# Kernel optimization log

Hardware: AMD Instinct MI355X
Metric: run time of the kernel (lower is better)

## Reference

```python
import jax, jax.numpy as jnp
import numpy as np

B, D, H = 16, 512, 8
MA, MR = 2048, 256  # padded max atoms / residues per graph
EPS = 1e-5


def _counts():
    ca = 1024 + (np.arange(B) * 97) % 1024   # atoms per graph
    cr = 128 + (np.arange(B) * 37) % 128     # residues per graph
    return ca, cr


def to_dense(x, batch, M):
    """PyG to_dense_batch: flat [N, D] + sorted batch ids -> [B, M, D] padded + mask."""
    N = x.shape[0]
    counts = jax.ops.segment_sum(jnp.ones(N, jnp.int32), batch, num_segments=B)
    starts = jnp.concatenate([jnp.zeros(1, counts.dtype), jnp.cumsum(counts)[:-1]])
    pos = jnp.arange(N, dtype=jnp.int32) - starts[batch]
    dense = jnp.zeros((B, M, x.shape[1]), x.dtype).at[batch, pos].set(x)
    mask = jnp.zeros((B, M), bool).at[batch, pos].set(True)
    return dense, mask, batch, pos


def mha(q, k, v, in_w, in_b, out_w, out_b, key_valid):
    """torch nn.MultiheadAttention (batch_first, eval) with key_padding_mask = ~key_valid."""
    Lq, Lk = q.shape[1], k.shape[1]
    dh = D // H
    wq, wk, wv = in_w[:D], in_w[D:2 * D], in_w[2 * D:]
    bq, bk, bv = in_b[:D], in_b[D:2 * D], in_b[2 * D:]
    qh = (q @ wq.T + bq).reshape(B, Lq, H, dh)
    kh = (k @ wk.T + bk).reshape(B, Lk, H, dh)
    vh = (v @ wv.T + bv).reshape(B, Lk, H, dh)
    scores = jnp.einsum('bqhd,bkhd->bhqk', qh, kh) / jnp.sqrt(jnp.asarray(dh, q.dtype))
    scores = jnp.where(key_valid[:, None, None, :], scores, jnp.asarray(-1e9, scores.dtype))
    attn = jax.nn.softmax(scores, axis=-1)
    out = jnp.einsum('bhqk,bkhd->bqhd', attn, vh).reshape(B, Lq, D)
    return out @ out_w.T + out_b


def layernorm(x, g, b):
    m = x.mean(-1, keepdims=True)
    v = ((x - m) ** 2).mean(-1, keepdims=True)
    return (x - m) * jax.lax.rsqrt(v + EPS) * g + b


def setup_inputs() -> dict:
    key = jax.random.key(0)
    ks = jax.random.split(key, 8)
    ca, cr = _counts()
    Na, Nr = int(ca.sum()), int(cr.sum())
    s = 0.02
    return {
        'atom_node': jax.random.normal(ks[0], (Na, D), jnp.float32),
        'res_node': jax.random.normal(ks[1], (Nr, D), jnp.float32),
        'r2a_in_w': jax.random.normal(ks[2], (3 * D, D), jnp.float32) * s,
        'r2a_in_b': jnp.zeros((3 * D,), jnp.float32),
        'r2a_out_w': jax.random.normal(ks[3], (D, D), jnp.float32) * s,
        'r2a_out_b': jnp.zeros((D,), jnp.float32),
        'a2r_in_w': jax.random.normal(ks[4], (3 * D, D), jnp.float32) * s,
        'a2r_in_b': jnp.zeros((3 * D,), jnp.float32),
        'a2r_out_w': jax.random.normal(ks[5], (D, D), jnp.float32) * s,
        'a2r_out_b': jnp.zeros((D,), jnp.float32),
        'atom_ln_g': jnp.ones((D,), jnp.float32),
        'atom_ln_b': jnp.zeros((D,), jnp.float32),
        'res_ln_g': jnp.ones((D,), jnp.float32),
        'res_ln_b': jnp.zeros((D,), jnp.float32),
        'atom_batch': jnp.asarray(np.repeat(np.arange(B), ca), jnp.int32),
        'res_batch': jnp.asarray(np.repeat(np.arange(B), cr), jnp.int32),
    }


def reference(atom_node, res_node, r2a_in_w, r2a_in_b, r2a_out_w, r2a_out_b,
              a2r_in_w, a2r_in_b, a2r_out_w, a2r_out_b,
              atom_ln_g, atom_ln_b, res_ln_g, res_ln_b,
              atom_batch, res_batch):
    atom_d, atom_mask, ab, ap = to_dense(atom_node, atom_batch, MA)
    res_d, res_mask, rb, rp = to_dense(res_node, res_batch, MR)
    # res2atom: atoms attend over residues; atom2res: residues attend over (updated) atoms
    atom_upd = mha(atom_d, res_d, res_d, r2a_in_w, r2a_in_b, r2a_out_w, r2a_out_b, res_mask)
    res_upd = mha(res_d, atom_upd, atom_upd, a2r_in_w, a2r_in_b, a2r_out_w, a2r_out_b, atom_mask)
    atom_out = layernorm(atom_upd, atom_ln_g, atom_ln_b)[ab, ap] + atom_node
    res_out = layernorm(res_upd, res_ln_g, res_ln_b)[rb, rp] + res_node
    return atom_out, res_out
```

## Files before the change

kernel.cpp:

```cpp
#include <hip/hip_runtime.h>
#include <hip/hip_bf16.h>
#include <math.h>

#define DD 512
#define NA_TOT 22904
#define NR_TOT 2904
#define MPAD_A 22960
#define MPAD_R 2960

__constant__ int c_aoff[17] = {0,1024,2145,3363,4678,6090,7599,9205,10908,12708,
                               14605,16599,17666,18830,20091,21449,22904};
__constant__ int c_roff[17] = {0,128,293,495,734,882,1067,1289,1420,1588,
                               1793,2035,2186,2374,2599,2733,2904};
__constant__ int c_apad[17] = {0,1024,2152,3376,4696,6112,7624,9232,10936,12736,
                               14640,16640,17712,18880,20144,21504,22960};
__constant__ int c_rpad[17] = {0,128,296,504,744,896,1088,1312,1448,1616,
                               1824,2072,2224,2416,2648,2784,2960};

typedef __attribute__((ext_vector_type(8))) short short8;
typedef __attribute__((ext_vector_type(4))) float f32x4;
typedef __attribute__((ext_vector_type(4))) unsigned short ushort4v;

__device__ __forceinline__ unsigned short f2bf(float f) {
  __hip_bfloat16 h = __float2bfloat16(f);
  return *reinterpret_cast<unsigned short*>(&h);
}
__device__ __forceinline__ float bf2f(unsigned short u) {
  union { unsigned int i; float f; } c; c.i = ((unsigned int)u) << 16; return c.f;
}
__device__ __forceinline__ float wred_sum(float x){
#pragma unroll
  for (int o = 32; o > 0; o >>= 1) x += __shfl_xor(x, o, 64);
  return x;
}

__device__ __forceinline__ void gl_lds16(const unsigned short* g, unsigned short* l) {
  __builtin_amdgcn_global_load_lds(
      (const __attribute__((address_space(1))) unsigned int*)g,
      (__attribute__((address_space(3))) unsigned int*)l, 16, 0, 0);
}

__global__ __launch_bounds__(256) void cvt5(
    const float* __restrict__ s0, const float* __restrict__ s1,
    const float* __restrict__ s2, const float* __restrict__ s3,
    const float* __restrict__ s4,
    unsigned short* __restrict__ d0, unsigned short* __restrict__ d1,
    unsigned short* __restrict__ d2, unsigned short* __restrict__ d3,
    unsigned short* __restrict__ d4,
    int n0, int n1, int n2, int n3, int n4)
{
  const float* s; unsigned short* d; int n;
  switch (blockIdx.y) {
    case 0: s = s0; d = d0; n = n0; break;
    case 1: s = s1; d = d1; n = n1; break;
    case 2: s = s2; d = d2; n = n2; break;
    case 3: s = s3; d = d3; n = n3; break;
    default: s = s4; d = d4; n = n4; break;
  }
  const int i = (blockIdx.x * 256 + threadIdx.x) * 4;
  if (i < n) {
    const float4 v = *reinterpret_cast<const float4*>(s + i);
    ushort4v o = { f2bf(v.x), f2bf(v.y), f2bf(v.z), f2bf(v.w) };
    *reinterpret_cast<ushort4v*>(d + i) = o;
  }
}

__global__ __launch_bounds__(256) void cvt_atom(const float* __restrict__ s,
                                                unsigned short* __restrict__ d, int n)
{
  const int i = (blockIdx.x * 256 + threadIdx.x) * 8;
  if (i < n) {
    const float4 v0 = *reinterpret_cast<const float4*>(s + i);
    const float4 v1 = *reinterpret_cast<const float4*>(s + i + 4);
    short8 pk;
    pk[0] = (short)f2bf(v0.x); pk[1] = (short)f2bf(v0.y);
    pk[2] = (short)f2bf(v0.z); pk[3] = (short)f2bf(v0.w);
    pk[4] = (short)f2bf(v1.x); pk[5] = (short)f2bf(v1.y);
    pk[6] = (short)f2bf(v1.z); pk[7] = (short)f2bf(v1.w);
    *reinterpret_cast<short8*>(d + i) = pk;
  }
}

__global__ __launch_bounds__(256) void mkmap(int* __restrict__ mapA,
                                             int* __restrict__ mapR)
{
  const int pm = blockIdx.x * 256 + threadIdx.x;
  if (pm < MPAD_A) {
    int b = 0;
#pragma unroll
    for (int i = 1; i < 16; ++i) if (pm >= c_apad[i]) b = i;
    const int rel = pm - c_apad[b];
    const int L = c_aoff[b+1] - c_aoff[b];
    mapA[pm] = c_aoff[b] + min(rel, L - 1);
  }
  if (pm < MPAD_R) {
    int b = 0;
#pragma unroll
    for (int i = 1; i < 16; ++i) if (pm >= c_rpad[i]) b = i;
    const int rel = pm - c_rpad[b];
    const int L = c_roff[b+1] - c_roff[b];
    mapR[pm] = c_roff[b] + min(rel, L - 1);
  }
}

struct GSeg {
  const void* X; const unsigned short* W; const float* bias;
  unsigned short* Y; const int* map;
  int M; int ldY; int mtiles; int flags;
};
struct GSeg4 { GSeg s[4]; };

__global__ __launch_bounds__(256) void gemm_multi(GSeg4 P, int mtpx)
{
  __shared__ unsigned short SMEM[40960];
  unsigned short* const Xb0 = SMEM;
  unsigned short* const Xb1 = SMEM + 8192;
  unsigned short* const Xb2 = SMEM + 16384;
  unsigned short* const Wb0 = SMEM + 24576;
  unsigned short* const Wb1 = SMEM + 32768;
  const GSeg sg = P.s[blockIdx.y];
  const int xcd = blockIdx.x & 7, g = blockIdx.x >> 3;
  const int mt = xcd + 8 * (g % mtpx);
  const int nt = g / mtpx;
  if (mt >= sg.mtiles) return;
  const int m0 = mt * 128, n0 = nt * 128;
  const int OUTT = sg.flags & 2, REMAP = sg.flags & 4;
  const int tid = threadIdx.x, lane = tid & 63, w = tid >> 6;
  const int la = lane & 15, lg = lane >> 4;
  const int wm = (w & 1) * 64, wn = (w >> 1) * 64;
  const int w64 = w * 64;
  const unsigned short* Xg = (const unsigned short*)sg.X;

  f32x4 acc[4][4];
#pragma unroll
  for (int i = 0; i < 4; ++i)
#pragma unroll
    for (int j = 0; j < 4; ++j) acc[i][j] = (f32x4){0.f,0.f,0.f,0.f};

  int elA[4][2], elB[4][2];
#pragma unroll
  for (int i = 0; i < 4; ++i)
#pragma unroll
    for (int kc = 0; kc < 2; ++kc) {
      { const int r = wm + i*16 + la;
        elA[i][kc] = r*64 + ((kc*32 + lg*8) ^ ((r & 7) << 3)); }
      { const int r = wn + i*16 + la;
        elB[i][kc] = r*64 + ((kc*32 + lg*8) ^ ((r & 7) << 3)); }
    }

  int srow[4];
#pragma unroll
  for (int p = 0; p < 4; ++p) {
    const int slot = p*256 + tid;
    const int rg = min(m0 + (slot >> 3), sg.M - 1);
    srow[p] = REMAP ? sg.map[rg] : rg;
  }
  int scg[4], srw[4];
#pragma unroll
  for (int p = 0; p < 4; ++p) {
    const int slot = p*256 + tid;
    srw[p] = slot >> 3;
    scg[p] = ((slot & 7) ^ (srw[p] & 7)) << 3;
  }

#define STAGE_W(DST, kb_)                                                       \
  _Pragma("unroll")                                                             \
  for (int p = 0; p < 4; ++p)                                                   \
    gl_lds16(sg.W + (size_t)(n0 + srw[p]) * DD + (kb_) + scg[p],                \
             &(DST)[(p*256 + w64) * 8]);

#define STAGE_X(DST, kb_)                                                       \
  _Pragma("unroll")                                                             \
  for (int p = 0; p < 4; ++p)                                                   \
    gl_lds16(Xg + (size_t)srow[p] * DD + (kb_) + scg[p],                        \
             &(DST)[(p*256 + w64) * 8]);

#define COMPUTE(XB, WB)                                                         \
  {                                                                             \
    short8 af[4][2], bfm[4][2];                                                 \
    _Pragma("unroll")                                                           \
    for (int i = 0; i < 4; ++i)                                                 \
      _Pragma("unroll")                                                         \
      for (int kc = 0; kc < 2; ++kc) {                                          \
        af[i][kc]  = *reinterpret_cast<const short8*>(&(XB)[elA[i][kc]]);       \
        bfm[i][kc] = *reinterpret_cast<const short8*>(&(WB)[elB[i][kc]]);       \
      }                                                                         \
    _Pragma("unroll")                                                           \
    for (int kc = 0; kc < 2; ++kc)                                              \
      _Pragma("unroll")                                                         \
      for (int i = 0; i < 4; ++i)                                               \
        _Pragma("unroll")                                                       \
        for (int j = 0; j < 4; ++j)                                             \
          acc[i][j] = __builtin_amdgcn_mfma_f32_16x16x32_bf16(af[i][kc], bfm[j][kc], acc[i][j], 0, 0, 0); \
  }

  STAGE_W(Wb0, 0);
  STAGE_X(Xb0, 0);
  STAGE_X(Xb1, 64);

#pragma unroll
  for (int k = 0; k < 8; ++k) {
    __builtin_amdgcn_s_barrier();
    asm volatile("" ::: "memory");
    if (k + 1 < 8) {
      if (((k+1) & 1) == 0) { STAGE_W(Wb0, (k+1)*64); } else { STAGE_W(Wb1, (k+1)*64); }
    }
    if (k + 2 < 8) {
      if (((k+2) % 3) == 0) { STAGE_X(Xb0, (k+2)*64); }
      else if (((k+2) % 3) == 1) { STAGE_X(Xb1, (k+2)*64); }
      else { STAGE_X(Xb2, (k+2)*64); }
    }
    if (k < 6)       { asm volatile("s_waitcnt vmcnt(12)" ::: "memory"); }
    else if (k == 6) { asm volatile("s_waitcnt vmcnt(8)" ::: "memory"); }
    else             { asm volatile("s_waitcnt vmcnt(0)" ::: "memory"); }
    __builtin_amdgcn_s_barrier();
    asm volatile("" ::: "memory");
    __builtin_amdgcn_sched_barrier(0);
    if ((k % 3) == 0)      { if ((k & 1) == 0) COMPUTE(Xb0, Wb0) else COMPUTE(Xb0, Wb1) }
    else if ((k % 3) == 1) { if ((k & 1) == 0) COMPUTE(Xb1, Wb0) else COMPUTE(Xb1, Wb1) }
    else                   { if ((k & 1) == 0) COMPUTE(Xb2, Wb0) else COMPUTE(Xb2, Wb1) }
  }

#undef STAGE_W
#undef STAGE_X
#undef COMPUTE

  __syncthreads();
  unsigned short* Cs = SMEM;
  if (!OUTT) {
#pragma unroll
    for (int j = 0; j < 4; ++j) {
      const int n = wn + j*16 + la;
      const float bj = sg.bias[n0 + n];
#pragma unroll
      for (int i = 0; i < 4; ++i) {
        const int mb = wm + i*16 + lg*4;
#pragma unroll
        for (int r = 0; r < 4; ++r) {
          const int m = mb + r;
          Cs[m*128 + (((n >> 3) ^ (m & 7)) << 3) + (n & 7)] = f2bf(acc[i][j][r] + bj);
        }
      }
    }
    __syncthreads();
#pragma unroll
    for (int p = 0; p < 8; ++p) {
      const int sid = p*256 + tid;
      const int row = sid >> 4, s = sid & 15;
      if (m0 + row < sg.M) {
        const short8 v = *reinterpret_cast<const short8*>(&Cs[row*128 + ((s ^ (row & 7)) << 3)]);
        *reinterpret_cast<short8*>(sg.Y + (size_t)(m0 + row)*sg.ldY + n0 + s*8) = v;
      }
    }
  } else {
#pragma unroll
    for (int j = 0; j < 4; ++j) {
      const int n = wn + j*16 + la;
      const float bj = sg.bias[n0 + n];
#pragma unroll
      for (int i = 0; i < 4; ++i) {
        const int mb = wm + i*16 + lg*4;
#pragma unroll
        for (int r = 0; r < 4; ++r) {
          const int m = mb + r;
          Cs[n*128 + (((m >> 3) ^ (n & 7)) << 3) + (m & 7)] = f2bf(acc[i][j][r] + bj);
        }
      }
    }
    __syncthreads();
#pragma unroll
    for (int p = 0; p < 8; ++p) {
      const int sid = p*256 + tid;
      const int row = sid >> 4, s = sid & 15;
      if (m0 + s*8 < sg.M) {
        const short8 v = *reinterpret_cast<const short8*>(&Cs[row*128 + ((s ^ (row & 7)) << 3)]);
        *reinterpret_cast<short8*>(sg.Y + (size_t)(n0 + row)*sg.ldY + m0 + s*8) = v;
      }
    }
  }
}

#define ATT_STAGE(bi, kc_)                                                      \
  {                                                                             \
    const int kbase_ = (kc_) * 64;                                              \
    _Pragma("unroll")                                                           \
    for (int p = 0; p < 2; ++p) {                                               \
      const int slot = p*256 + tid;                                             \
      const int row = slot >> 3, cg = slot & 7;                                 \
      const int srow = min(kbase_ + row, padL - 1);                             \
      gl_lds16(Kb + (size_t)srow * DD + ((cg ^ (row & 7)) << 3),                \
               &Ks[bi][(p*256 + w*64) * 8]);                                    \
    }                                                                           \
    _Pragma("unroll")                                                           \
    for (int p = 0; p < 2; ++p) {                                               \
      const int slot = p*256 + tid;                                             \
      const int row = slot >> 3, cg = slot & 7;                                 \
      const int col = min(kbase_ + ((cg ^ (row & 7)) << 3), padL - 8);          \
      gl_lds16(VTb + (size_t)row * ldvt + col, &Vs[bi][(p*256 + w*64) * 8]);    \
    }                                                                           \
  }

#define ATT_COMPUTE(bi, kbase)                                                  \
  {                                                                             \
    f32x4 S[4];                                                                 \
    _Pragma("unroll")                                                           \
    for (int j = 0; j < 4; ++j) {                                               \
      const int row = j*16 + la;                                                \
      const short8 kf0 = *reinterpret_cast<const short8*>(                      \
          &Ks[bi][row*64 + ((lg*8) ^ ((row & 7) << 3))]);                       \
      const short8 kf1 = *reinterpret_cast<const short8*>(                      \
          &Ks[bi][row*64 + ((32 + lg*8) ^ ((row & 7) << 3))]);                  \
      f32x4 s = (f32x4){0.f,0.f,0.f,0.f};                                       \
      s = __builtin_amdgcn_mfma_f32_16x16x32_bf16(qf[0], kf0, s, 0, 0, 0);      \
      s = __builtin_amdgcn_mfma_f32_16x16x32_bf16(qf[1], kf1, s, 0, 0, 0);      \
      S[j] = s;                                                                 \
    }                                                                           \
    _Pragma("unroll")                                                           \
    for (int j = 0; j < 4; ++j) {                                               \
      const bool ok = (kbase + j*16 + la) < Lk;                                 \
      _Pragma("unroll")                                                         \
      for (int r = 0; r < 4; ++r) {                                             \
        const float p = ok ? __expf(S[j][r] * 0.125f) : 0.f;                    \
        S[j][r] = p;                                                            \
        lsum[r] += p;                                                           \
      }                                                                         \
    }                                                                           \
    _Pragma("unroll")                                                           \
    for (int r = 0; r < 4; ++r) {                                               \
      const int prow = lg*4 + r;                                                \
      _Pragma("unroll")                                                         \
      for (int j = 0; j < 4; ++j)                                               \
        Pl[w][prow*64 + ((j*16 + la) ^ ((prow & 7) << 3))] = f2bf(S[j][r]);     \
    }                                                                           \
    __builtin_amdgcn_wave_barrier();                                            \
    const short8 pf0 = *reinterpret_cast<const short8*>(                        \
        &Pl[w][la*64 + ((lg*8) ^ ((la & 7) << 3))]);                            \
    const short8 pf1 = *reinterpret_cast<const short8*>(                        \
        &Pl[w][la*64 + ((32 + lg*8) ^ ((la & 7) << 3))]);                       \
    _Pragma("unroll")                                                           \
    for (int j = 0; j < 4; ++j) {                                               \
      const int d = j*16 + la;                                                  \
      const short8 vf0 = *reinterpret_cast<const short8*>(                      \
          &Vs[bi][d*64 + ((lg*8) ^ ((d & 7) << 3))]);                           \
      const short8 vf1 = *reinterpret_cast<const short8*>(                      \
          &Vs[bi][d*64 + ((32 + lg*8) ^ ((d & 7) << 3))]);                      \
      acc[j] = __builtin_amdgcn_mfma_f32_16x16x32_bf16(pf0, vf0, acc[j], 0, 0, 0); \
      acc[j] = __builtin_amdgcn_mfma_f32_16x16x32_bf16(pf1, vf1, acc[j], 0, 0, 0); \
    }                                                                           \
  }

__global__ __launch_bounds__(256, 4) void attn_v7(const unsigned short* __restrict__ Q,
                                                  const unsigned short* __restrict__ K,
                                                  const unsigned short* __restrict__ VT,
                                                  unsigned short* __restrict__ O, int ldvt)
{
  __shared__ unsigned short Ks[2][64*64];
  __shared__ unsigned short Vs[2][64*64];
  __shared__ unsigned short Pl[4][16*64];
  const int b = blockIdx.x >> 3, h = blockIdx.x & 7;
  const int Lq = c_aoff[b+1]-c_aoff[b], Lk = c_roff[b+1]-c_roff[b];
  const int padL = c_rpad[b+1]-c_rpad[b];
  const int q0b = blockIdx.y * 64;
  if (q0b >= Lq) return;
  const int tid = threadIdx.x, w = tid >> 6, lane = tid & 63;
  const int la = lane & 15, lg = lane >> 4;
  const int q0 = q0b + w*16;
  const unsigned short* Qb  = Q  + (size_t)c_aoff[b]*DD + h*64;
  const unsigned short* Kb  = K  + (size_t)c_rpad[b]*DD + h*64;
  const unsigned short* VTb = VT + (size_t)(h*64)*ldvt + c_rpad[b];

  short8 qf[2];
  {
    const int qrow = min(q0 + la, Lq - 1);
    qf[0] = *reinterpret_cast<const short8*>(Qb + (size_t)qrow*DD + lg*8);
    qf[1] = *reinterpret_cast<const short8*>(Qb + (size_t)qrow*DD + 32 + lg*8);
  }

  f32x4 acc[4];
#pragma unroll
  for (int j = 0; j < 4; ++j) acc[j] = (f32x4){0.f,0.f,0.f,0.f};
  float lsum[4] = {0.f,0.f,0.f,0.f};

  const int nkc = (Lk + 63) >> 6;
  ATT_STAGE(0, 0);
  for (int kc = 0; kc < nkc; ++kc) {
    const int bi = kc & 1;
    __builtin_amdgcn_s_barrier();
    asm volatile("" ::: "memory");
    if (kc + 1 < nkc) {
      ATT_STAGE(bi ^ 1, kc + 1);
      asm volatile("s_waitcnt vmcnt(4)" ::: "memory");
    } else {
      asm volatile("s_waitcnt vmcnt(0)" ::: "memory");
    }
    __builtin_amdgcn_s_barrier();
    asm volatile("" ::: "memory");
    __builtin_amdgcn_sched_barrier(0);
    const int kbase = kc * 64;
    ATT_COMPUTE(bi, kbase);
  }

#pragma unroll
  for (int msk = 1; msk <= 8; msk <<= 1)
#pragma unroll
    for (int r = 0; r < 4; ++r) lsum[r] += __shfl_xor(lsum[r], msk, 64);

#pragma unroll
  for (int r = 0; r < 4; ++r) {
    const float inv = 1.f / lsum[r];
    const int prow = lg*4 + r;
#pragma unroll
    for (int j = 0; j < 4; ++j)
      Pl[w][prow*64 + ((j*16 + la) ^ ((prow & 7) << 3))] = f2bf(acc[j][r] * inv);
  }
  __builtin_amdgcn_wave_barrier();
#pragma unroll
  for (int p = 0; p < 2; ++p) {
    const int sid = p*64 + lane;
    const int row = sid >> 3, s = sid & 7;
    const int qrow = q0 + row;
    if (qrow < Lq) {
      const short8 v = *reinterpret_cast<const short8*>(
          &Pl[w][row*64 + ((s ^ (row & 7)) << 3)]);
      *reinterpret_cast<short8*>(O + (size_t)(c_aoff[b] + qrow)*DD + h*64 + s*8) = v;
    }
  }
}

__global__ __launch_bounds__(256, 4) void attn_sk(const unsigned short* __restrict__ Q,
                                                  const unsigned short* __restrict__ K,
                                                  const unsigned short* __restrict__ VT,
                                                  float* __restrict__ Pout)
{
  __shared__ unsigned short Ks[2][64*64];
  __shared__ unsigned short Vs[2][64*64];
  __shared__ unsigned short Pl[4][16*64];
  const int b = blockIdx.x >> 3, h = blockIdx.x & 7;
  const int qt = blockIdx.y, z = blockIdx.z;
  const int Lq = c_roff[b+1]-c_roff[b], Lk = c_aoff[b+1]-c_aoff[b];
  const int padL = c_apad[b+1]-c_apad[b];
  const int ldvt = MPAD_A;
  const int q0b = qt * 64;
  if (q0b >= Lq) return;
  const int tid = threadIdx.x, w = tid >> 6, lane = tid & 63;
  const int la = lane & 15, lg = lane >> 4;
  const int q0 = q0b + w*16;
  float* pp = Pout + ((size_t)(blockIdx.x*4 + qt)*4 + z) * 4160;

  const int nkc = (Lk + 63) >> 6;
  const int cps = (nkc + 3) >> 2;
  const int k0 = z * cps, k1 = min(k0 + cps, nkc);
  if (k0 >= k1) {
    for (int i = tid; i < 4160; i += 256) pp[i] = 0.f;
    return;
  }

  const unsigned short* Qb  = Q  + (size_t)c_roff[b]*DD + h*64;
  const unsigned short* Kb  = K  + (size_t)c_apad[b]*DD + h*64;
  const unsigned short* VTb = VT + (size_t)(h*64)*ldvt + c_apad[b];

  short8 qf[2];
  {
    const int qrow = min(q0 + la, Lq - 1);
    qf[0] = *reinterpret_cast<const short8*>(Qb + (size_t)qrow*DD + lg*8);
    qf[1] = *reinterpret_cast<const short8*>(Qb + (size_t)qrow*DD + 32 + lg*8);
  }

  f32x4 acc[4];
#pragma unroll
  for (int j = 0; j < 4; ++j) acc[j] = (f32x4){0.f,0.f,0.f,0.f};
  float lsum[4] = {0.f,0.f,0.f,0.f};

  ATT_STAGE(0, k0);
  for (int kc = k0; kc < k1; ++kc) {
    const int bi = (kc - k0) & 1;
    __builtin_amdgcn_s_barrier();
    asm volatile("" ::: "memory");
    if (kc + 1 < k1) {
      ATT_STAGE(bi ^ 1, kc + 1);
      asm volatile("s_waitcnt vmcnt(4)" ::: "memory");
    } else {
      asm volatile("s_waitcnt vmcnt(0)" ::: "memory");
    }
    __builtin_amdgcn_s_barrier();
    asm volatile("" ::: "memory");
    __builtin_amdgcn_sched_barrier(0);
    const int kbase = kc * 64;
    ATT_COMPUTE(bi, kbase);
  }

#pragma unroll
  for (int msk = 1; msk <= 8; msk <<= 1)
#pragma unroll
    for (int r = 0; r < 4; ++r) lsum[r] += __shfl_xor(lsum[r], msk, 64);

#pragma unroll
  for (int j = 0; j < 4; ++j)
#pragma unroll
    for (int r = 0; r < 4; ++r)
      pp[(size_t)(w*16 + lg*4 + r)*64 + j*16 + la] = acc[j][r];
  if (la == 0) {
#pragma unroll
    for (int r = 0; r < 4; ++r) pp[4096 + w*16 + lg*4 + r] = lsum[r];
  }
}

__global__ __launch_bounds__(256) void attn_red(const float* __restrict__ Pin,
                                                unsigned short* __restrict__ O)
{
  const int b = blockIdx.x >> 3, h = blockIdx.x & 7;
  const int qt = blockIdx.y;
  const int Lq = c_roff[b+1]-c_roff[b];
  const int q0b = qt * 64;
  if (q0b >= Lq) return;
  const int t = threadIdx.x;
  const int row = t >> 2, dg = (t & 3) * 16;
  if (q0b + row >= Lq) return;
  const float* base = Pin + ((size_t)(blockIdx.x*4 + qt)*4) * 4160;
  const float ls = base[4096 + row] + base[4160 + 4096 + row]
                 + base[2*4160 + 4096 + row] + base[3*4160 + 4096 + row];
  const float inv = 1.f / ls;
  unsigned short ov[16];
#pragma unroll
  for (int e = 0; e < 16; ++e) {
    const int idx = row*64 + dg + e;
    const float s = base[idx] + base[4160 + idx] + base[2*4160 + idx] + base[3*4160 + idx];
    ov[e] = f2bf(s * inv);
  }
  unsigned short* dst = O + (size_t)(c_roff[b] + q0b + row)*DD + h*64 + dg;
  *reinterpret_cast<short8*>(dst)     = *reinterpret_cast<short8*>(&ov[0]);
  *reinterpret_cast<short8*>(dst + 8) = *reinterpret_cast<short8*>(&ov[8]);
}

__global__ __launch_bounds__(256) void ln_res(const unsigned short* __restrict__ Ub,
    float* __restrict__ Yout,
    const float* __restrict__ atom_node, const float* __restrict__ res_node,
    const float* __restrict__ ag, const float* __restrict__ ab,
    const float* __restrict__ rg, const float* __restrict__ rb)
{
  const int row = blockIdx.x * 4 + (threadIdx.x >> 6);
  const int lane = threadIdx.x & 63;
  if (row >= NA_TOT + NR_TOT) return;
  const float* g; const float* bb; const float* resid;
  if (row < NA_TOT) { g = ag; bb = ab; resid = atom_node + (size_t)row * DD; }
  else { g = rg; bb = rb; resid = res_node + (size_t)(row - NA_TOT) * DD; }
  const short8 xb = *reinterpret_cast<const short8*>(Ub + (size_t)row*DD + lane*8);
  float xv[8];
#pragma unroll
  for (int i = 0; i < 8; ++i) xv[i] = bf2f((unsigned short)xb[i]);
  float s = 0.f;
#pragma unroll
  for (int i = 0; i < 8; ++i) s += xv[i];
  s = wred_sum(s);
  const float mean = s * (1.f/512.f);
  float vs = 0.f;
#pragma unroll
  for (int i = 0; i < 8; ++i) { const float d = xv[i] - mean; vs = fmaf(d, d, vs); }
  vs = wred_sum(vs) * (1.f/512.f);
  const float inv = rsqrtf(vs + 1e-5f);
  const float4 g0 = *reinterpret_cast<const float4*>(g + lane*8);
  const float4 g1 = *reinterpret_cast<const float4*>(g + lane*8 + 4);
  const float4 b0 = *reinterpret_cast<const float4*>(bb + lane*8);
  const float4 b1 = *reinterpret_cast<const float4*>(bb + lane*8 + 4);
  const float4 r0 = *reinterpret_cast<const float4*>(resid + lane*8);
  const float4 r1 = *reinterpret_cast<const float4*>(resid + lane*8 + 4);
  float4 o0, o1;
  o0.x = (xv[0]-mean)*inv*g0.x + b0.x + r0.x;
  o0.y = (xv[1]-mean)*inv*g0.y + b0.y + r0.y;
  o0.z = (xv[2]-mean)*inv*g0.z + b0.z + r0.z;
  o0.w = (xv[3]-mean)*inv*g0.w + b0.w + r0.w;
  o1.x = (xv[4]-mean)*inv*g1.x + b1.x + r1.x;
  o1.y = (xv[5]-mean)*inv*g1.y + b1.y + r1.y;
  o1.z = (xv[6]-mean)*inv*g1.z + b1.z + r1.z;
  o1.w = (xv[7]-mean)*inv*g1.w + b1.w + r1.w;
  float* y = Yout + (size_t)row * DD + lane*8;
  *reinterpret_cast<float4*>(y)     = o0;
  *reinterpret_cast<float4*>(y + 4) = o1;
}

extern "C" void kernel_launch(void* const* d_in, const int* in_sizes, int n_in,
                              void* d_out, int out_size, void* d_ws, size_t ws_size,
                              hipStream_t stream) {
  (void)in_sizes; (void)n_in; (void)out_size; (void)ws_size;
  const float* atom_node = (const float*)d_in[0];
  const float* res_node  = (const float*)d_in[1];
  const float* r2a_in_w  = (const float*)d_in[2];
  const float* r2a_in_b  = (const float*)d_in[3];
  const float* r2a_out_w = (const float*)d_in[4];
  const float* r2a_out_b = (const float*)d_in[5];
  const float* a2r_in_w  = (const float*)d_in[6];
  const float* a2r_in_b  = (const float*)d_in[7];
  const float* a2r_out_w = (const float*)d_in[8];
  const float* a2r_out_b = (const float*)d_in[9];
  const float* atom_ln_g = (const float*)d_in[10];
  const float* atom_ln_b = (const float*)d_in[11];
  const float* res_ln_g  = (const float*)d_in[12];
  const float* res_ln_b  = (const float*)d_in[13];

  float* out = (float*)d_out;
  unsigned short* wsb = (unsigned short*)d_ws;
  const size_t NAD = (size_t)NA_TOT * DD;
  const size_t NRD = (size_t)NR_TOT * DD;
  const size_t PAD = (size_t)MPAD_A * DD;
  const size_t PRD = (size_t)MPAD_R * DD;
  unsigned short* slab1  = wsb;
  unsigned short* slab2  = wsb + PAD;
  unsigned short* updb   = wsb + 2*PAD;
  unsigned short* res_bf = wsb + 2*PAD + NAD + NRD;
  unsigned short* K1     = res_bf + NRD;
  unsigned short* V1T    = K1 + PRD;
  unsigned short* Q2     = V1T + PRD;
  unsigned short* O2     = Q2 + NRD;
  unsigned short* wbf    = O2 + NRD;
  unsigned short* w_r2a_in  = wbf;
  unsigned short* w_r2a_out = wbf +  786432;
  unsigned short* w_a2r_in  = wbf + 1048576;
  unsigned short* w_a2r_out = wbf + 1835008;
  int* mapA = (int*)(wbf + 2097152);
  int* mapR = mapA + MPAD_A;
  unsigned short* Q1      = slab1;
  unsigned short* atom_bf = slab2;
  unsigned short* O1      = slab2;
  unsigned short* K2      = slab1;
  unsigned short* V2T     = slab2;
  float* partials = out;

  const dim3 blk(256);

  mkmap<<<dim3((MPAD_A + 255)/256), blk, 0, stream>>>(mapA, mapR);
  cvt5<<<dim3(1452, 5), blk, 0, stream>>>(
      r2a_in_w, r2a_out_w, a2r_in_w, a2r_out_w, res_node,
      w_r2a_in, w_r2a_out, w_a2r_in, w_a2r_out, res_bf,
      786432, 262144, 786432, 262144, (int)NRD);
  cvt_atom<<<dim3((int)(NAD/2048)), blk, 0, stream>>>(atom_node, atom_bf, (int)NAD);

  {
    GSeg4 A;
    A.s[0] = { atom_bf, w_r2a_in,          r2a_in_b,        Q1,  nullptr, NA_TOT, 512,    179, 0 };
    A.s[1] = { res_bf,  w_r2a_in + 262144, r2a_in_b + 512,  K1,  mapR,    MPAD_R, 512,    24,  4 };
    A.s[2] = { res_bf,  w_r2a_in + 524288, r2a_in_b + 1024, V1T, mapR,    MPAD_R, MPAD_R, 24,  6 };
    A.s[3] = { res_bf,  w_a2r_in,          a2r_in_b,        Q2,  nullptr, NR_TOT, 512,    23,  0 };
    gemm_multi<<<dim3(736, 4), blk, 0, stream>>>(A, 23);
  }
  attn_v7<<<dim3(128, 32), blk, 0, stream>>>(Q1, K1, V1T, O1, MPAD_R);
  {
    GSeg4 B;
    B.s[0] = { O1, w_r2a_out, r2a_out_b, updb, nullptr, NA_TOT, 512, 179, 0 };
    B.s[1] = B.s[0]; B.s[2] = B.s[0]; B.s[3] = B.s[0];
    gemm_multi<<<dim3(736, 1), blk, 0, stream>>>(B, 23);
  }
  {
    GSeg4 C;
    C.s[0] = { updb, w_a2r_in + 262144, a2r_in_b + 512,  K2,  mapA, MPAD_A, 512,    180, 4 };
    C.s[1] = { updb, w_a2r_in + 524288, a2r_in_b + 1024, V2T, mapA, MPAD_A, MPAD_A, 180, 6 };
    C.s[2] = C.s[0]; C.s[3] = C.s[0];
    gemm_multi<<<dim3(736, 2), blk, 0, stream>>>(C, 23);
  }
  attn_sk<<<dim3(128, 4, 4), blk, 0, stream>>>(Q2, K2, V2T, partials);
  attn_red<<<dim3(128, 4), blk, 0, stream>>>(partials, O2);
  {
    GSeg4 E;
    E.s[0] = { O2, w_a2r_out, a2r_out_b, updb + NAD, nullptr, NR_TOT, 512, 23, 0 };
    E.s[1] = E.s[0]; E.s[2] = E.s[0]; E.s[3] = E.s[0];
    gemm_multi<<<dim3(96, 1), blk, 0, stream>>>(E, 3);
  }
  ln_res<<<dim3((NA_TOT + NR_TOT + 3) / 4), blk, 0, stream>>>(
      updb, out, atom_node, res_node, atom_ln_g, atom_ln_b, res_ln_g, res_ln_b);
}
```

Before: 212.6 us.

## Fold out-projection into atom2res K/V weights to fuse dependent GEMMs

Precomputes combined weights Wk·Wo and Wv·Wo (plus folded biases) in fp32, then bf16, so K2 and V2T are computed directly from the attention output O1. This lets the out-projection GEMM and the K/V projection GEMMs run in a single launch instead of two dependent ones, removing a serial stage and the re-read of updb. It adds small per-call weight-combine kernels, an extra workspace slab for V2T, and rounds the fused weights to bf16, which may change numerics slightly compared with projecting the rounded updb.

```diff
diff --git a/kernel.cpp b/kernel.cpp
--- a/kernel.cpp
+++ b/kernel.cpp
@@ -101,6 +101,60 @@
     const int L = c_roff[b+1] - c_roff[b];
     mapR[pm] = c_roff[b] + min(rel, L - 1);
   }
+}
+
+__global__ __launch_bounds__(256) void wcomb(const float* __restrict__ a2r_in_w,
+                                             const float* __restrict__ Wo,
+                                             unsigned short* __restrict__ Ck,
+                                             unsigned short* __restrict__ Cv)
+{
+  __shared__ float As[32][36];
+  __shared__ float Bs[32][36];
+  const float* A = a2r_in_w + (blockIdx.z ? 524288 : 262144);
+  unsigned short* C = blockIdx.z ? Cv : Ck;
+  const int m0 = blockIdx.x * 32, n0 = blockIdx.y * 32;
+  const int tid = threadIdx.x;
+  const int ty = tid >> 4, tx = tid & 15;
+  const int lr = tid >> 3, lc = (tid & 7) * 4;
+  float acc[2][2] = {{0.f,0.f},{0.f,0.f}};
+  for (int kb = 0; kb < 512; kb += 32) {
+    const float4 av = *reinterpret_cast<const float4*>(A + (size_t)(m0+lr)*512 + kb + lc);
+    As[lr][lc+0]=av.x; As[lr][lc+1]=av.y; As[lr][lc+2]=av.z; As[lr][lc+3]=av.w;
+    const float4 bv = *reinterpret_cast<const float4*>(Wo + (size_t)(kb+lr)*512 + n0 + lc);
+    Bs[lr][lc+0]=bv.x; Bs[lr][lc+1]=bv.y; Bs[lr][lc+2]=bv.z; Bs[lr][lc+3]=bv.w;
+    __syncthreads();
+#pragma unroll
+    for (int k = 0; k < 32; ++k) {
+      const float a0 = As[ty*2][k],   a1 = As[ty*2+1][k];
+      const float b0 = Bs[k][tx*2],   b1 = Bs[k][tx*2+1];
+      acc[0][0] = fmaf(a0,b0,acc[0][0]); acc[0][1] = fmaf(a0,b1,acc[0][1]);
+      acc[1][0] = fmaf(a1,b0,acc[1][0]); acc[1][1] = fmaf(a1,b1,acc[1][1]);
+    }
+    __syncthreads();
+  }
+#pragma unroll
+  for (int i = 0; i < 2; ++i)
+#pragma unroll
+    for (int j = 0; j < 2; ++j)
+      C[(size_t)(m0+ty*2+i)*512 + n0 + tx*2+j] = f2bf(acc[i][j]);
+}
+
+__global__ __launch_bounds__(256) void bcomb(const float* __restrict__ a2r_in_w,
+                                             const float* __restrict__ bo,
+                                             const float* __restrict__ a2r_in_b,
+                                             float* __restrict__ bck,
+                                             float* __restrict__ bcv)
+{
+  const int n = blockIdx.x * 256 + threadIdx.x;
+  const float* A  = a2r_in_w + (blockIdx.y ? 524288 : 262144) + (size_t)n * 512;
+  const float* b2 = a2r_in_b + (blockIdx.y ? 1024 : 512);
+  float s = 0.f;
+  for (int j = 0; j < 512; j += 4) {
+    const float4 w = *reinterpret_cast<const float4*>(A + j);
+    const float4 b = *reinterpret_cast<const float4*>(bo + j);
+    s = fmaf(w.x,b.x,s); s = fmaf(w.y,b.y,s); s = fmaf(w.z,b.z,s); s = fmaf(w.w,b.w,s);
+  }
+  (blockIdx.y ? bcv : bck)[n] = s + b2[n];
 }
 
 struct GSeg {
@@ -508,7 +562,8 @@
 __global__ __launch_bounds__(256) void attn_red(const float* __restrict__ Pin,
                                                 unsigned short* __restrict__ O)
 {
-  const int b = blockIdx.x >> 3, h = blockIdx.x & 7;
+  const int b = blockIdx.x >> 3;
+  const int h = blockIdx.x & 7;
   const int qt = blockIdx.y;
   const int Lq = c_roff[b+1]-c_roff[b];
   const int q0b = qt * 64;
@@ -605,8 +660,9 @@
   const size_t PRD = (size_t)MPAD_R * DD;
   unsigned short* slab1  = wsb;
   unsigned short* slab2  = wsb + PAD;
-  unsigned short* updb   = wsb + 2*PAD;
-  unsigned short* res_bf = wsb + 2*PAD + NAD + NRD;
+  unsigned short* slab3  = wsb + 2*PAD;
+  unsigned short* updb   = wsb + 3*PAD;
+  unsigned short* res_bf = updb + NAD + NRD;
   unsigned short* K1     = res_bf + NRD;
   unsigned short* V1T    = K1 + PRD;
   unsigned short* Q2     = V1T + PRD;
@@ -618,12 +674,16 @@
   unsigned short* w_a2r_out = wbf + 1835008;
   int* mapA = (int*)(wbf + 2097152);
   int* mapR = mapA + MPAD_A;
+  unsigned short* wc_k = (unsigned short*)(mapR + MPAD_R);
+  unsigned short* wc_v = wc_k + 262144;
+  float* bc_k = (float*)(wc_v + 262144);
+  float* bc_v = bc_k + 512;
+  float* partials = (float*)(bc_v + 512);
   unsigned short* Q1      = slab1;
   unsigned short* atom_bf = slab2;
   unsigned short* O1      = slab2;
   unsigned short* K2      = slab1;
-  unsigned short* V2T     = slab2;
-  float* partials = out;
+  unsigned short* V2T     = slab3;
 
   const dim3 blk(256);
 
@@ -633,6 +693,8 @@
       w_r2a_in, w_r2a_out, w_a2r_in, w_a2r_out, res_bf,
       786432, 262144, 786432, 262144, (int)NRD);
   cvt_atom<<<dim3((int)(NAD/2048)), blk, 0, stream>>>(atom_node, atom_bf, (int)NAD);
+  wcomb<<<dim3(16, 16, 2), blk, 0, stream>>>(a2r_in_w, r2a_out_w, wc_k, wc_v);
+  bcomb<<<dim3(2, 2), blk, 0, stream>>>(a2r_in_w, r2a_out_b, a2r_in_b, bc_k, bc_v);
 
   {
     GSeg4 A;
@@ -645,16 +707,11 @@
   attn_v7<<<dim3(128, 32), blk, 0, stream>>>(Q1, K1, V1T, O1, MPAD_R);
   {
     GSeg4 B;
-    B.s[0] = { O1, w_r2a_out, r2a_out_b, updb, nullptr, NA_TOT, 512, 179, 0 };
-    B.s[1] = B.s[0]; B.s[2] = B.s[0]; B.s[3] = B.s[0];
-    gemm_multi<<<dim3(736, 1), blk, 0, stream>>>(B, 23);
-  }
-  {
-    GSeg4 C;
-    C.s[0] = { updb, w_a2r_in + 262144, a2r_in_b + 512,  K2,  mapA, MPAD_A, 512,    180, 4 };
-    C.s[1] = { updb, w_a2r_in + 524288, a2r_in_b + 1024, V2T, mapA, MPAD_A, MPAD_A, 180, 6 };
-    C.s[2] = C.s[0]; C.s[3] = C.s[0];
-    gemm_multi<<<dim3(736, 2), blk, 0, stream>>>(C, 23);
+    B.s[0] = { O1, w_r2a_out, r2a_out_b, updb, nullptr, NA_TOT, 512,    179, 0 };
+    B.s[1] = { O1, wc_k,      bc_k,      K2,   mapA,    MPAD_A, 512,    180, 4 };
+    B.s[2] = { O1, wc_v,      bc_v,      V2T,  mapA,    MPAD_A, MPAD_A, 180, 6 };
+    B.s[3] = B.s[0];
+    gemm_multi<<<dim3(736, 3), blk, 0, stream>>>(B, 23);
   }
   attn_sk<<<dim3(128, 4, 4), blk, 0, stream>>>(Q2, K2, V2T, partials);
   attn_red<<<dim3(128, 4), blk, 0, stream>>>(partials, O2);
```

New measurement: 241.2 us. 13.4% more time.
